# Kernel tuning notes

Measured on AMD Instinct MI355X. Metric: run time of the kernel, lower is better.

Reference implementation:

```python
import jax, jax.numpy as jnp
import numpy as np

NUM_CLASSES = 10


def setup_inputs() -> dict:
    key = jax.random.key(0)
    k1, k2, k3 = jax.random.split(key, 3)
    N, M, D = 1024, 50000, 512
    x = jax.random.normal(k1, (N, D), dtype=jnp.float32)
    exemplars = jax.random.normal(k2, (M, D), dtype=jnp.float32)
    labels = jax.random.randint(k3, (M,), 0, NUM_CLASSES)
    Sigma_inv = jnp.ones((D,), dtype=jnp.float32)
    beta = jnp.ones((1,), dtype=jnp.float32)
    gamma = jnp.ones((1,), dtype=jnp.float32)
    return {"x": x, "exemplars": exemplars, "labels": labels,
            "Sigma_inv": Sigma_inv, "beta": beta, "gamma": gamma}


def reference(x, exemplars, labels, Sigma_inv, beta, gamma):
    # Weighted squared Mahalanobis distance via expanded quadratic form:
    # dist[n,m] = sum_d Sigma_inv[d] * (x[n,d] - e[m,d])^2
    #           = (x^2 @ S) + (e^2 @ S) - 2 * (x*S) @ e^T
    x_sq = jnp.einsum('nd,d->n', x * x, Sigma_inv)            # [N]
    e_sq = jnp.einsum('md,d->m', exemplars * exemplars, Sigma_inv)  # [M]
    cross = jnp.einsum('nd,md->nm', x * Sigma_inv, exemplars)  # [N, M]
    distances = x_sq[:, None] + e_sq[None, :] - 2.0 * cross    # [N, M]
    attention = jnp.exp(-beta[0] * distances)                  # [N, M]
    # Per-class masked sum == segment sum over exemplar labels.
    logits = jax.ops.segment_sum(attention.T, labels,
                                 num_segments=NUM_CLASSES).T   # [N, 10]
    return jax.nn.softmax(gamma[0] * logits, axis=1)
```

## Files before the change

kernel.cpp:

```cpp
#include <hip/hip_runtime.h>
#include <hip/hip_bf16.h>
#include <stdint.h>
#include <stddef.h>

#define N_TOT 1024
#define M_TOT 50000
#define M_PAD 50048
#define D_TOT 512
#define NC    10

typedef __attribute__((ext_vector_type(8))) __bf16 bf16x8;
typedef __attribute__((ext_vector_type(4))) float f32x4;
typedef __attribute__((ext_vector_type(4))) unsigned int u32x4;

union Frag16 { u32x4 q; bf16x8 b; unsigned short u[8]; };
union Pack8  { u32x4 q; unsigned short u[8]; };

__device__ __forceinline__ unsigned short f2bf(float x) {
  unsigned int u = __float_as_uint(x);
  unsigned int r = (u + 0x7fffu + ((u >> 16) & 1u)) >> 16;
  return (unsigned short)r;
}

__device__ __forceinline__ void gld_lds16(const void* g, void* l) {
  auto gp = (__attribute__((address_space(1))) unsigned int*)(uintptr_t)g;
  auto lp = (__attribute__((address_space(3))) unsigned int*)(uintptr_t)l;
  __builtin_amdgcn_global_load_lds(gp, lp, 16, 0, 0);
}

__global__ void prep_rows(const float* __restrict__ e, const float* __restrict__ x,
                          const float* __restrict__ S,
                          unsigned short* __restrict__ eb, unsigned short* __restrict__ xb,
                          float* __restrict__ e_sq, float* __restrict__ x_sq) {
  const int lane = threadIdx.x & 63;
  const int wid  = threadIdx.x >> 6;
  const int row  = blockIdx.x * 4 + wid;
  const int d0   = lane * 8;

  float4 s0 = *(const float4*)(S + d0);
  float4 s1 = *(const float4*)(S + d0 + 4);
  float ss[8] = {s0.x, s0.y, s0.z, s0.w, s1.x, s1.y, s1.z, s1.w};

  float acc = 0.f;
  Pack8 o;

  if (row < M_PAD) {
    if (row < M_TOT) {
      const float* src = e + (size_t)row * D_TOT + d0;
      float4 v0 = *(const float4*)src;
      float4 v1 = *(const float4*)(src + 4);
      float vv[8] = {v0.x, v0.y, v0.z, v0.w, v1.x, v1.y, v1.z, v1.w};
      #pragma unroll
      for (int j = 0; j < 8; ++j) { acc += ss[j] * vv[j] * vv[j]; o.u[j] = f2bf(vv[j]); }
    } else {
      #pragma unroll
      for (int j = 0; j < 8; ++j) o.u[j] = 0;
      acc = 0.f;
    }
    *(u32x4*)(eb + (size_t)row * D_TOT + d0) = o.q;
    #pragma unroll
    for (int off = 32; off; off >>= 1) acc += __shfl_down(acc, off);
    if (lane == 0) e_sq[row] = (row < M_TOT) ? acc : 1e30f;
  } else {
    const int xr = row - M_PAD;
    const float* src = x + (size_t)xr * D_TOT + d0;
    float4 v0 = *(const float4*)src;
    float4 v1 = *(const float4*)(src + 4);
    float vv[8] = {v0.x, v0.y, v0.z, v0.w, v1.x, v1.y, v1.z, v1.w};
    #pragma unroll
    for (int j = 0; j < 8; ++j) {
      float w = ss[j] * vv[j];
      acc += w * vv[j];
      o.u[j] = f2bf(w);
    }
    *(u32x4*)(xb + (size_t)xr * D_TOT + d0) = o.q;
    #pragma unroll
    for (int off = 32; off; off >>= 1) acc += __shfl_down(acc, off);
    if (lane == 0) x_sq[xr] = acc;
  }
}

__global__ void zero_f32(float* __restrict__ p, int n) {
  int i = blockIdx.x * 256 + threadIdx.x;
  if (i < n) p[i] = 0.f;
}

__launch_bounds__(256)
__global__ void gemm_fused(const unsigned short* __restrict__ xb,
                           const unsigned short* __restrict__ eb,
                           const float* __restrict__ x_sq, const float* __restrict__ e_sq,
                           const int* __restrict__ labels,
                           const float* __restrict__ betap,
                           float* __restrict__ logits) {
  __shared__ unsigned short As[128 * 32];
  __shared__ unsigned short Bs[128 * 32];
  __shared__ float cls[128 * NC];

  const int tid  = threadIdx.x;
  const int lane = tid & 63;
  const int wid  = tid >> 6;
  const int wr   = wid >> 1, wc = wid & 1;
  const int mt   = blockIdx.x;
  const int nt   = blockIdx.y;

  const int rA0   = tid >> 2;
  const int colu0 = (tid & 3) * 8;
  const unsigned short* gA0 = xb + (size_t)(nt * 128 + rA0) * D_TOT + colu0;
  const unsigned short* gA1 = gA0 + (size_t)64 * D_TOT;
  const unsigned short* gB0 = eb + (size_t)(mt * 128 + rA0) * D_TOT + colu0;
  const unsigned short* gB1 = gB0 + (size_t)64 * D_TOT;
  unsigned short* lA0 = As + tid * 8;
  unsigned short* lA1 = As + (tid + 256) * 8;
  unsigned short* lB0 = Bs + tid * 8;
  unsigned short* lB1 = Bs + (tid + 256) * 8;

  const f32x4 vzero = {0.f, 0.f, 0.f, 0.f};
  f32x4 acc[4][4];
  #pragma unroll
  for (int i = 0; i < 4; ++i)
    #pragma unroll
    for (int j = 0; j < 4; ++j) acc[i][j] = vzero;

  const int arow = wr * 64 + (lane & 15);
  const int brow = wc * 64 + (lane & 15);
  const int koff = (lane >> 4) * 8;

  for (int ks = 0; ks < 16; ++ks) {
    const int k0 = ks * 32;
    __syncthreads();
    gld_lds16(gA0 + k0, lA0);
    gld_lds16(gA1 + k0, lA1);
    gld_lds16(gB0 + k0, lB0);
    gld_lds16(gB1 + k0, lB1);
    __syncthreads();

    Frag16 fa[4], fb[4];
    #pragma unroll
    for (int i = 0; i < 4; ++i) fa[i].q = *(const u32x4*)(As + (arow + i * 16) * 32 + koff);
    #pragma unroll
    for (int j = 0; j < 4; ++j) fb[j].q = *(const u32x4*)(Bs + (brow + j * 16) * 32 + koff);
    #pragma unroll
    for (int i = 0; i < 4; ++i)
      #pragma unroll
      for (int j = 0; j < 4; ++j)
        acc[i][j] = __builtin_amdgcn_mfma_f32_16x16x32_bf16(fa[i].b, fb[j].b, acc[i][j], 0, 0, 0);
  }

  __syncthreads();
  for (int t = tid; t < 128 * NC; t += 256) cls[t] = 0.f;
  __syncthreads();

  const float beta = betap[0];
  const int mbase = mt * 128 + wc * 64 + (lane & 15);
  int   lab[4]; float esq[4]; bool mv[4];
  #pragma unroll
  for (int j = 0; j < 4; ++j) {
    const int m = mbase + j * 16;
    mv[j]  = (m < M_TOT);
    esq[j] = e_sq[m];
    lab[j] = mv[j] ? labels[m] : 0;
  }

  #pragma unroll
  for (int i = 0; i < 4; ++i) {
    #pragma unroll
    for (int r = 0; r < 4; ++r) {
      const int nloc = wr * 64 + i * 16 + (lane >> 4) * 4 + r;
      const float xs = x_sq[nt * 128 + nloc];
      #pragma unroll
      for (int j = 0; j < 4; ++j) {
        if (!mv[j]) continue;
        const float dist = xs + esq[j] - 2.0f * acc[i][j][r];
        const float a = __expf(-beta * dist);
        if (a != 0.0f) atomicAdd(&cls[nloc * NC + lab[j]], a);
      }
    }
  }
  __syncthreads();
  for (int t = tid; t < 128 * NC; t += 256) {
    const float v = cls[t];
    if (v != 0.0f) atomicAdd(&logits[(size_t)(nt * 128 + (t / NC)) * NC + (t % NC)], v);
  }
}

__global__ void softmax_out(const float* __restrict__ logits,
                            const float* __restrict__ gammap,
                            float* __restrict__ out) {
  const int n = blockIdx.x * blockDim.x + threadIdx.x;
  if (n >= N_TOT) return;
  const float g = gammap[0];
  float v[NC], mx = -3.4e38f;
  #pragma unroll
  for (int c = 0; c < NC; ++c) { v[c] = g * logits[n * NC + c]; mx = fmaxf(mx, v[c]); }
  float s = 0.f;
  #pragma unroll
  for (int c = 0; c < NC; ++c) { v[c] = __expf(v[c] - mx); s += v[c]; }
  const float inv = 1.0f / s;
  #pragma unroll
  for (int c = 0; c < NC; ++c) out[n * NC + c] = v[c] * inv;
}

extern "C" void kernel_launch(void* const* d_in, const int* in_sizes, int n_in,
                              void* d_out, int out_size, void* d_ws, size_t ws_size,
                              hipStream_t stream) {
  const float* x      = (const float*)d_in[0];
  const float* e      = (const float*)d_in[1];
  const int*   labels = (const int*)d_in[2];
  const float* S      = (const float*)d_in[3];
  const float* beta   = (const float*)d_in[4];
  const float* gamma  = (const float*)d_in[5];

  char* ws = (char*)d_ws;
  unsigned short* eb     = (unsigned short*)(ws);
  unsigned short* xb     = (unsigned short*)(ws + 51249152);
  float*          e_sq   = (float*)(ws + 52297728);
  float*          x_sq   = (float*)(ws + 52497920);
  float*          logits = (float*)(ws + 52502016);

  hipLaunchKernelGGL(prep_rows, dim3((M_PAD + N_TOT) / 4), dim3(256), 0, stream,
                     e, x, S, eb, xb, e_sq, x_sq);
  hipLaunchKernelGGL(zero_f32, dim3(40), dim3(256), 0, stream, logits, N_TOT * NC);
  hipLaunchKernelGGL(gemm_fused, dim3(391, 8), dim3(256), 0, stream,
                     xb, eb, x_sq, e_sq, labels, beta, logits);
  hipLaunchKernelGGL(softmax_out, dim3(4), dim3(256), 0, stream,
                     logits, gamma, (float*)d_out);
}
```

Baseline: 258.0 us.

## Double-buffer LDS tiles in fused GEMM and swap grid order for reuse

```diff
diff --git a/kernel.cpp b/kernel.cpp
--- a/kernel.cpp
+++ b/kernel.cpp
@@ -92,27 +92,23 @@
                            const int* __restrict__ labels,
                            const float* __restrict__ betap,
                            float* __restrict__ logits) {
-  __shared__ unsigned short As[128 * 32];
-  __shared__ unsigned short Bs[128 * 32];
+  __shared__ unsigned short As[2][128 * 32];
+  __shared__ unsigned short Bs[2][128 * 32];
   __shared__ float cls[128 * NC];
 
   const int tid  = threadIdx.x;
   const int lane = tid & 63;
   const int wid  = tid >> 6;
   const int wr   = wid >> 1, wc = wid & 1;
-  const int mt   = blockIdx.x;
-  const int nt   = blockIdx.y;
-
-  const int rA0   = tid >> 2;
-  const int colu0 = (tid & 3) * 8;
-  const unsigned short* gA0 = xb + (size_t)(nt * 128 + rA0) * D_TOT + colu0;
-  const unsigned short* gA1 = gA0 + (size_t)64 * D_TOT;
-  const unsigned short* gB0 = eb + (size_t)(mt * 128 + rA0) * D_TOT + colu0;
-  const unsigned short* gB1 = gB0 + (size_t)64 * D_TOT;
-  unsigned short* lA0 = As + tid * 8;
-  unsigned short* lA1 = As + (tid + 256) * 8;
-  unsigned short* lB0 = Bs + tid * 8;
-  unsigned short* lB1 = Bs + (tid + 256) * 8;
+  const int nt   = blockIdx.x;
+  const int mt   = blockIdx.y;
+
+  const int cA0 = wid * 128 + lane;
+  const int cA1 = cA0 + 64;
+  const unsigned short* gA0 = xb + (size_t)(nt * 128 + (cA0 >> 2)) * D_TOT + (cA0 & 3) * 8;
+  const unsigned short* gA1 = xb + (size_t)(nt * 128 + (cA1 >> 2)) * D_TOT + (cA1 & 3) * 8;
+  const unsigned short* gB0 = eb + (size_t)(mt * 128 + (cA0 >> 2)) * D_TOT + (cA0 & 3) * 8;
+  const unsigned short* gB1 = eb + (size_t)(mt * 128 + (cA1 >> 2)) * D_TOT + (cA1 & 3) * 8;
 
   const f32x4 vzero = {0.f, 0.f, 0.f, 0.f};
   f32x4 acc[4][4];
@@ -125,26 +121,50 @@
   const int brow = wc * 64 + (lane & 15);
   const int koff = (lane >> 4) * 8;
 
-  for (int ks = 0; ks < 16; ++ks) {
-    const int k0 = ks * 32;
-    __syncthreads();
-    gld_lds16(gA0 + k0, lA0);
-    gld_lds16(gA1 + k0, lA1);
-    gld_lds16(gB0 + k0, lB0);
-    gld_lds16(gB1 + k0, lB1);
-    __syncthreads();
-
-    Frag16 fa[4], fb[4];
-    #pragma unroll
-    for (int i = 0; i < 4; ++i) fa[i].q = *(const u32x4*)(As + (arow + i * 16) * 32 + koff);
-    #pragma unroll
-    for (int j = 0; j < 4; ++j) fb[j].q = *(const u32x4*)(Bs + (brow + j * 16) * 32 + koff);
-    #pragma unroll
-    for (int i = 0; i < 4; ++i)
-      #pragma unroll
-      for (int j = 0; j < 4; ++j)
-        acc[i][j] = __builtin_amdgcn_mfma_f32_16x16x32_bf16(fa[i].b, fb[j].b, acc[i][j], 0, 0, 0);
-  }
+  #define STAGE(BUF, K0)                                    \
+    do {                                                    \
+      gld_lds16(gA0 + (K0), &As[(BUF)][cA0 * 8]);           \
+      gld_lds16(gA1 + (K0), &As[(BUF)][cA1 * 8]);           \
+      gld_lds16(gB0 + (K0), &Bs[(BUF)][cA0 * 8]);           \
+      gld_lds16(gB1 + (K0), &Bs[(BUF)][cA1 * 8]);           \
+    } while (0)
+
+  #define COMPUTE(BUF)                                                            \
+    do {                                                                          \
+      Frag16 fa[4], fb[4];                                                        \
+      _Pragma("unroll")                                                           \
+      for (int i = 0; i < 4; ++i)                                                 \
+        fa[i].q = *(const u32x4*)(&As[(BUF)][(arow + i * 16) * 32 + koff]);       \
+      _Pragma("unroll")                                                           \
+      for (int j = 0; j < 4; ++j)                                                 \
+        fb[j].q = *(const u32x4*)(&Bs[(BUF)][(brow + j * 16) * 32 + koff]);       \
+      _Pragma("unroll")                                                           \
+      for (int i = 0; i < 4; ++i)                                                 \
+        _Pragma("unroll")                                                         \
+        for (int j = 0; j < 4; ++j)                                               \
+          acc[i][j] = __builtin_amdgcn_mfma_f32_16x16x32_bf16(fa[i].b, fb[j].b,   \
+                                                              acc[i][j], 0, 0, 0);\
+    } while (0)
+
+  STAGE(0, 0);
+  #pragma unroll 2
+  for (int ks = 0; ks < 15; ++ks) {
+    const int cur = ks & 1;
+    STAGE(cur ^ 1, (ks + 1) * 32);
+    asm volatile("s_waitcnt vmcnt(4)" ::: "memory");
+    __builtin_amdgcn_s_barrier();
+    asm volatile("" ::: "memory");
+    COMPUTE(cur);
+    asm volatile("s_waitcnt lgkmcnt(0)" ::: "memory");
+    __builtin_amdgcn_sched_barrier(0);
+    __builtin_amdgcn_s_barrier();
+  }
+  asm volatile("s_waitcnt vmcnt(0)" ::: "memory");
+  __builtin_amdgcn_s_barrier();
+  asm volatile("" ::: "memory");
+  COMPUTE(1);
+  #undef STAGE
+  #undef COMPUTE
 
   __syncthreads();
   for (int t = tid; t < 128 * NC; t += 256) cls[t] = 0.f;
@@ -220,7 +240,7 @@
   hipLaunchKernelGGL(prep_rows, dim3((M_PAD + N_TOT) / 4), dim3(256), 0, stream,
                      e, x, S, eb, xb, e_sq, x_sq);
   hipLaunchKernelGGL(zero_f32, dim3(40), dim3(256), 0, stream, logits, N_TOT * NC);
-  hipLaunchKernelGGL(gemm_fused, dim3(391, 8), dim3(256), 0, stream,
+  hipLaunchKernelGGL(gemm_fused, dim3(8, 391), dim3(256), 0, stream,
                      xb, eb, x_sq, e_sq, labels, beta, logits);
   hipLaunchKernelGGL(softmax_out, dim3(4), dim3(256), 0, stream,
                      logits, gamma, (float*)d_out);
```

After: 247.9 us. 1.04x faster.
